# Optimization experiments

Hardware: AMD Instinct MI355X
Metric: run time of the kernel (lower is better)

## Reference

```python
import jax, jax.numpy as jnp
import numpy as np
from jax import lax

WS = 7  # window_size
PAD = WS // 2


def _gaussian_window(window_size, channel, sigma=1.5):
    x = np.arange(window_size, dtype=np.float64)
    g = np.exp(-((x - window_size // 2) ** 2) / (2.0 * sigma ** 2))
    g = g / g.sum()
    w2 = np.outer(g, g).astype(np.float32)  # (ws, ws)
    w = np.broadcast_to(w2[None, None], (channel, 1, window_size, window_size))
    return jnp.asarray(np.ascontiguousarray(w))


def setup_inputs() -> dict:
    key = jax.random.key(0)
    k1, k2, k3 = jax.random.split(key, 3)
    shape = (16, 1, 1024, 1024)
    img1 = jax.random.uniform(k1, shape, dtype=jnp.float32)
    img2 = jax.random.uniform(k2, shape, dtype=jnp.float32)
    img3 = jax.random.uniform(k3, shape, dtype=jnp.float32)
    window = _gaussian_window(WS, channel=1)  # (1,1,7,7) depthwise Gaussian
    return {"img1": img1, "img2": img2, "img3": img3, "window": window}


def _dwconv(x, window, channel):
    # depthwise conv2d, SAME-style padding = ws//2, groups = channel
    return lax.conv_general_dilated(
        x, window, window_strides=(1, 1), padding=[(PAD, PAD), (PAD, PAD)],
        dimension_numbers=("NCHW", "OIHW", "NCHW"), feature_group_count=channel)


def reference(img1, img2, img3, window):
    channel = img1.shape[1]
    conv = lambda x: _dwconv(x, window, channel)

    mu1 = conv(img1)
    mu2 = conv(img2)
    mu3 = conv(img3)

    sigma1_sq = conv(img1 * img1) - mu1 * mu1
    sigma2_sq = conv(img2 * img2) - mu2 * mu2
    sigma3_sq = conv(img3 * img3) - mu3 * mu3
    sigma12 = conv(img1 * img2) - mu1 * mu2
    sigma13 = conv(img1 * img3) - mu1 * mu3

    C2 = 0.03 ** 2
    ssim_map_12 = (2.0 * sigma12 + C2) / (sigma1_sq + sigma2_sq + C2)
    ssim_map_13 = (2.0 * sigma13 + C2) / (sigma1_sq + sigma3_sq + C2)

    # size_average=True branch
    ssim_map = jnp.where(mu2 > mu3, ssim_map_12, ssim_map_13)
    return jnp.mean(ssim_map)
```

## Files before the change

kernel.cpp:

```cpp
#include <hip/hip_runtime.h>

typedef float v2f __attribute__((ext_vector_type(2)));

#define W 1024
#define H 1024
#define NB 16
#define TX 32
#define TY 18
#define HR 24
#define NTH 192
#define YBLK ((H + TY - 1) / TY)
#define RSTRIDE (8 * TX)

__global__ __launch_bounds__(NTH, 4) void ssim_main(
    const float* __restrict__ img1, const float* __restrict__ img2,
    const float* __restrict__ img3, const float* __restrict__ win,
    float* __restrict__ partial)
{
    __shared__ __align__(16) float hbuf[HR * RSTRIDE];
    __shared__ float wavesum[3];

    const int tid = threadIdx.x;
    const int x0  = blockIdx.x * TX;
    const int ys0 = blockIdx.y * TY;
    const size_t imoff = (size_t)blockIdx.z * (size_t)(W * H);
    const float* p1 = img1 + imoff;
    const float* p2 = img2 + imoff;
    const float* p3 = img3 + imoff;

    float g[7];
    {
        const float inv = 1.0f / sqrtf(win[24]);
        #pragma unroll
        for (int j = 0; j < 7; ++j) g[j] = win[21 + j] * inv;
    }

    {
        const int br  = tid >> 3;
        const int bc0 = (tid & 7) << 2;
        const int gy  = ys0 + br - 3;
        const int gx0 = x0 + bc0 - 4;
        const bool xfast = (gx0 >= 0) & (gx0 + 12 <= W);

        v2f accA[8], accB[8];
        #pragma unroll
        for (int ch = 0; ch < 8; ++ch) { accA[ch] = (v2f)0.0f; accB[ch] = (v2f)0.0f; }

        if ((gy >= 0) & (gy < H)) {
            const size_t rowoff = (size_t)gy * W;
            float V1[12], V2[12], V3[12];
            if (xfast) {
                const float* q1 = p1 + rowoff + gx0;
                const float* q2 = p2 + rowoff + gx0;
                const float* q3 = p3 + rowoff + gx0;
                *(float4*)&V1[0] = *(const float4*)(q1);
                *(float4*)&V1[4] = *(const float4*)(q1 + 4);
                *(float4*)&V1[8] = *(const float4*)(q1 + 8);
                *(float4*)&V2[0] = *(const float4*)(q2);
                *(float4*)&V2[4] = *(const float4*)(q2 + 4);
                *(float4*)&V2[8] = *(const float4*)(q2 + 8);
                *(float4*)&V3[0] = *(const float4*)(q3);
                *(float4*)&V3[4] = *(const float4*)(q3 + 4);
                *(float4*)&V3[8] = *(const float4*)(q3 + 8);
            } else {
                #pragma unroll
                for (int c = 0; c < 12; ++c) {
                    const int x = gx0 + c;
                    const bool ok = (x >= 0) & (x < W);
                    const size_t off = rowoff + x;
                    V1[c] = ok ? p1[off] : 0.0f;
                    V2[c] = ok ? p2[off] : 0.0f;
                    V3[c] = ok ? p3[off] : 0.0f;
                }
            }

            v2f gp[8];
            gp[0] = (v2f){g[0], 0.0f};
            #pragma unroll
            for (int m = 2; m <= 7; ++m) gp[m - 1] = (v2f){g[m - 1], g[m - 2]};
            gp[7] = (v2f){0.0f, g[6]};

            #pragma unroll
            for (int m = 1; m <= 8; ++m) {
                const v2f w = gp[m - 1];
                const float vA1 = V1[m], vA2 = V2[m], vA3 = V3[m];
                const float vB1 = V1[m + 2], vB2 = V2[m + 2], vB3 = V3[m + 2];
                v2f t;
                t = w * vA1; accA[0] += t; accA[3] += t * vA1; accA[6] += t * vA2; accA[7] += t * vA3;
                t = w * vA2; accA[1] += t; accA[4] += t * vA2;
                t = w * vA3; accA[2] += t; accA[5] += t * vA3;
                t = w * vB1; accB[0] += t; accB[3] += t * vB1; accB[6] += t * vB2; accB[7] += t * vB3;
                t = w * vB2; accB[1] += t; accB[4] += t * vB2;
                t = w * vB3; accB[2] += t; accB[5] += t * vB3;
            }
        }
        const int wbase = br * RSTRIDE + bc0;
        #pragma unroll
        for (int ch = 0; ch < 8; ++ch) {
            *(v2f*)&hbuf[wbase + ch * TX]     = accA[ch];
            *(v2f*)&hbuf[wbase + ch * TX + 2] = accB[ch];
        }
    }
    __syncthreads();

    const int tx = tid & 31;
    const int rg = tid >> 5;
    const int r0 = rg * 3;

    v2f s[4][3];
    #pragma unroll
    for (int cp = 0; cp < 4; ++cp)
        #pragma unroll
        for (int j = 0; j < 3; ++j) s[cp][j] = (v2f)0.0f;

    int base = r0 * RSTRIDE + tx;
    #pragma unroll
    for (int dy = 0; dy < 9; ++dy) {
        v2f p[4];
        #pragma unroll
        for (int cp = 0; cp < 4; ++cp) {
            p[cp].x = hbuf[base + cp * 64];
            p[cp].y = hbuf[base + cp * 64 + 32];
        }
        #pragma unroll
        for (int j = 0; j < 3; ++j) {
            const int dd = dy - j;
            if (dd >= 0 && dd < 7) {
                const float wg = g[dd];
                #pragma unroll
                for (int cp = 0; cp < 4; ++cp) s[cp][j] += wg * p[cp];
            }
        }
        base += RSTRIDE;
    }

    float lsum = 0.0f;
    #pragma unroll
    for (int j = 0; j < 3; ++j) {
        if (ys0 + r0 + j < H) {
            const float mu1 = s[0][j].x, mu2 = s[0][j].y;
            const float mu3 = s[1][j].x, E11 = s[1][j].y;
            const float E22 = s[2][j].x, E33 = s[2][j].y;
            const float E12 = s[3][j].x, E13 = s[3][j].y;
            const float sig1  = E11 - mu1 * mu1;
            const float sig2  = E22 - mu2 * mu2;
            const float sig3  = E33 - mu3 * mu3;
            const float sig12 = E12 - mu1 * mu2;
            const float sig13 = E13 - mu1 * mu3;
            const float C2 = 9.0e-4f;
            const float m12 = (2.0f * sig12 + C2) * __builtin_amdgcn_rcpf(sig1 + sig2 + C2);
            const float m13 = (2.0f * sig13 + C2) * __builtin_amdgcn_rcpf(sig1 + sig3 + C2);
            lsum += (mu2 > mu3) ? m12 : m13;
        }
    }

    #pragma unroll
    for (int o = 32; o > 0; o >>= 1) lsum += __shfl_down(lsum, o, 64);
    if ((tid & 63) == 0) wavesum[tid >> 6] = lsum;
    __syncthreads();
    if (tid == 0) {
        partial[((size_t)blockIdx.z * gridDim.y + blockIdx.y) * gridDim.x + blockIdx.x] =
            wavesum[0] + wavesum[1] + wavesum[2];
    }
}

__global__ __launch_bounds__(256) void ssim_reduce(
    const float* __restrict__ partial, float* __restrict__ out, int n)
{
    __shared__ double sh[256];
    const int tid = threadIdx.x;
    double s = 0.0;
    for (int i = tid; i < n; i += 256) s += (double)partial[i];
    sh[tid] = s;
    __syncthreads();
    for (int o = 128; o > 0; o >>= 1) {
        if (tid < o) sh[tid] += sh[tid + o];
        __syncthreads();
    }
    if (tid == 0) out[0] = (float)(sh[0] / (double)((size_t)NB * W * H));
}

extern "C" void kernel_launch(void* const* d_in, const int* in_sizes, int n_in,
                              void* d_out, int out_size, void* d_ws, size_t ws_size,
                              hipStream_t stream) {
    const float* img1 = (const float*)d_in[0];
    const float* img2 = (const float*)d_in[1];
    const float* img3 = (const float*)d_in[2];
    const float* win  = (const float*)d_in[3];
    float* out = (float*)d_out;
    float* partial = (float*)d_ws;

    dim3 grid(W / TX, YBLK, NB);
    ssim_main<<<grid, NTH, 0, stream>>>(img1, img2, img3, win, partial);

    const int nblk = (W / TX) * YBLK * NB;
    ssim_reduce<<<1, 256, 0, stream>>>(partial, out, nblk);
}
```

Measured before the change: 128.4 us.

## March blocks down a tall column strip, reusing the vertical halo across steps

Each block now handles a 32x128 strip in four 32-row steps instead of one 32x18 tile. It computes horizontal convolutions only for new rows and copies the 6-row halo inside shared memory between steps. This removes the heavy recomputation and reloading of halo rows: the old tiles spent 24 horizontal rows per 18 output rows, the new scheme about 38 per 128. The cost is extra syncs per step, a serial loop with less latency hiding, fewer blocks in the grid, and a larger shared buffer per block.

```diff
diff --git a/kernel.cpp b/kernel.cpp
--- a/kernel.cpp
+++ b/kernel.cpp
@@ -6,23 +6,81 @@
 #define H 1024
 #define NB 16
 #define TX 32
-#define TY 18
-#define HR 24
-#define NTH 192
-#define YBLK ((H + TY - 1) / TY)
+#define STEP 32
+#define NSTEP 4
+#define YSEG (STEP * NSTEP)
+#define BR 38
+#define NTH 256
 #define RSTRIDE (8 * TX)
+
+__device__ __forceinline__ void hconv_task(
+    const float* __restrict__ p1, const float* __restrict__ p2,
+    const float* __restrict__ p3, int gy, int gx0, bool xfast,
+    const v2f* __restrict__ gp, float* __restrict__ dst )
+{
+    v2f accA[8], accB[8];
+    #pragma unroll
+    for (int ch = 0; ch < 8; ++ch) { accA[ch] = (v2f)0.0f; accB[ch] = (v2f)0.0f; }
+
+    if ((gy >= 0) & (gy < H)) {
+        const size_t rowoff = (size_t)gy * W;
+        float V1[12], V2[12], V3[12];
+        if (xfast) {
+            const float* q1 = p1 + rowoff + gx0;
+            const float* q2 = p2 + rowoff + gx0;
+            const float* q3 = p3 + rowoff + gx0;
+            *(float4*)&V1[0] = *(const float4*)(q1);
+            *(float4*)&V1[4] = *(const float4*)(q1 + 4);
+            *(float4*)&V1[8] = *(const float4*)(q1 + 8);
+            *(float4*)&V2[0] = *(const float4*)(q2);
+            *(float4*)&V2[4] = *(const float4*)(q2 + 4);
+            *(float4*)&V2[8] = *(const float4*)(q2 + 8);
+            *(float4*)&V3[0] = *(const float4*)(q3);
+            *(float4*)&V3[4] = *(const float4*)(q3 + 4);
+            *(float4*)&V3[8] = *(const float4*)(q3 + 8);
+        } else {
+            #pragma unroll
+            for (int c = 0; c < 12; ++c) {
+                const int x = gx0 + c;
+                const bool ok = (x >= 0) & (x < W);
+                const size_t off = rowoff + x;
+                V1[c] = ok ? p1[off] : 0.0f;
+                V2[c] = ok ? p2[off] : 0.0f;
+                V3[c] = ok ? p3[off] : 0.0f;
+            }
+        }
+        #pragma unroll
+        for (int m = 1; m <= 8; ++m) {
+            const v2f w = gp[m - 1];
+            const float vA1 = V1[m], vA2 = V2[m], vA3 = V3[m];
+            const float vB1 = V1[m + 2], vB2 = V2[m + 2], vB3 = V3[m + 2];
+            v2f t;
+            t = w * vA1; accA[0] += t; accA[3] += t * vA1; accA[6] += t * vA2; accA[7] += t * vA3;
+            t = w * vA2; accA[1] += t; accA[4] += t * vA2;
+            t = w * vA3; accA[2] += t; accA[5] += t * vA3;
+            t = w * vB1; accB[0] += t; accB[3] += t * vB1; accB[6] += t * vB2; accB[7] += t * vB3;
+            t = w * vB2; accB[1] += t; accB[4] += t * vB2;
+            t = w * vB3; accB[2] += t; accB[5] += t * vB3;
+        }
+    }
+    #pragma unroll
+    for (int ch = 0; ch < 8; ++ch) {
+        *(v2f*)(dst + ch * TX)     = accA[ch];
+        *(v2f*)(dst + ch * TX + 2) = accB[ch];
+    }
+}
 
 __global__ __launch_bounds__(NTH, 4) void ssim_main(
     const float* __restrict__ img1, const float* __restrict__ img2,
     const float* __restrict__ img3, const float* __restrict__ win,
     float* __restrict__ partial)
 {
-    __shared__ __align__(16) float hbuf[HR * RSTRIDE];
-    __shared__ float wavesum[3];
+    __shared__ __align__(16) float hbuf[BR * RSTRIDE];
+    __shared__ float wavesum[4];
 
     const int tid = threadIdx.x;
     const int x0  = blockIdx.x * TX;
-    const int ys0 = blockIdx.y * TY;
+    const int ys0 = blockIdx.y * YSEG;
     const size_t imoff = (size_t)blockIdx.z * (size_t)(W * H);
     const float* p1 = img1 + imoff;
     const float* p2 = img2 + imoff;
@@ -34,114 +92,67 @@
         #pragma unroll
         for (int j = 0; j < 7; ++j) g[j] = win[21 + j] * inv;
     }
-
-    {
-        const int br  = tid >> 3;
-        const int bc0 = (tid & 7) << 2;
-        const int gy  = ys0 + br - 3;
-        const int gx0 = x0 + bc0 - 4;
-        const bool xfast = (gx0 >= 0) & (gx0 + 12 <= W);
-
-        v2f accA[8], accB[8];
-        #pragma unroll
-        for (int ch = 0; ch < 8; ++ch) { accA[ch] = (v2f)0.0f; accB[ch] = (v2f)0.0f; }
-
-        if ((gy >= 0) & (gy < H)) {
-            const size_t rowoff = (size_t)gy * W;
-            float V1[12], V2[12], V3[12];
-            if (xfast) {
-                const float* q1 = p1 + rowoff + gx0;
-                const float* q2 = p2 + rowoff + gx0;
-                const float* q3 = p3 + rowoff + gx0;
-                *(float4*)&V1[0] = *(const float4*)(q1);
-                *(float4*)&V1[4] = *(const float4*)(q1 + 4);
-                *(float4*)&V1[8] = *(const float4*)(q1 + 8);
-                *(float4*)&V2[0] = *(const float4*)(q2);
-                *(float4*)&V2[4] = *(const float4*)(q2 + 4);
-                *(float4*)&V2[8] = *(const float4*)(q2 + 8);
-                *(float4*)&V3[0] = *(const float4*)(q3);
-                *(float4*)&V3[4] = *(const float4*)(q3 + 4);
-                *(float4*)&V3[8] = *(const float4*)(q3 + 8);
-            } else {
-                #pragma unroll
-                for (int c = 0; c < 12; ++c) {
-                    const int x = gx0 + c;
-                    const bool ok = (x >= 0) & (x < W);
-                    const size_t off = rowoff + x;
-                    V1[c] = ok ? p1[off] : 0.0f;
-                    V2[c] = ok ? p2[off] : 0.0f;
-                    V3[c] = ok ? p3[off] : 0.0f;
+    v2f gp[8];
+    gp[0] = (v2f){g[0], 0.0f};
+    #pragma unroll
+    for (int m = 2; m <= 7; ++m) gp[m - 1] = (v2f){g[m - 1], g[m - 2]};
+    gp[7] = (v2f){0.0f, g[6]};
+
+    const int br  = tid >> 3;
+    const int bc0 = (tid & 7) << 2;
+    const int gx0 = x0 + bc0 - 4;
+    const bool xfast = (gx0 >= 0) & (gx0 + 12 <= W);
+
+    if (tid < 48) {
+        const int pr  = tid >> 3;
+        const int pc0 = (tid & 7) << 2;
+        const int pgx0 = x0 + pc0 - 4;
+        const bool pxf = (pgx0 >= 0) & (pgx0 + 12 <= W);
+        hconv_task(p1, p2, p3, ys0 - 3 + pr, pgx0, pxf, gp, &hbuf[pr * RSTRIDE + pc0]);
+    }
+
+    const int tx = tid & 31;
+    const int r0 = (tid >> 5) << 2;
+
+    float lsum = 0.0f;
+
+    for (int s = 0; s < NSTEP; ++s) {
+        hconv_task(p1, p2, p3, ys0 + s * STEP + 3 + br, gx0, xfast, gp,
+                   &hbuf[(6 + br) * RSTRIDE + bc0]);
+        __syncthreads();
+
+        v2f sv[4][4];
+        #pragma unroll
+        for (int cp = 0; cp < 4; ++cp)
+            #pragma unroll
+            for (int j = 0; j < 4; ++j) sv[cp][j] = (v2f)0.0f;
+
+        int base = r0 * RSTRIDE + tx;
+        #pragma unroll
+        for (int dy = 0; dy < 10; ++dy) {
+            v2f p[4];
+            #pragma unroll
+            for (int cp = 0; cp < 4; ++cp) {
+                p[cp].x = hbuf[base + cp * 64];
+                p[cp].y = hbuf[base + cp * 64 + 32];
+            }
+            #pragma unroll
+            for (int j = 0; j < 4; ++j) {
+                const int dd = dy - j;
+                if (dd >= 0 && dd < 7) {
+                    const float wg = g[dd];
+                    #pragma unroll
+                    for (int cp = 0; cp < 4; ++cp) sv[cp][j] += wg * p[cp];
                 }
             }
-
-            v2f gp[8];
-            gp[0] = (v2f){g[0], 0.0f};
-            #pragma unroll
-            for (int m = 2; m <= 7; ++m) gp[m - 1] = (v2f){g[m - 1], g[m - 2]};
-            gp[7] = (v2f){0.0f, g[6]};
-
-            #pragma unroll
-            for (int m = 1; m <= 8; ++m) {
-                const v2f w = gp[m - 1];
-                const float vA1 = V1[m], vA2 = V2[m], vA3 = V3[m];
-                const float vB1 = V1[m + 2], vB2 = V2[m + 2], vB3 = V3[m + 2];
-                v2f t;
-                t = w * vA1; accA[0] += t; accA[3] += t * vA1; accA[6] += t * vA2; accA[7] += t * vA3;
-                t = w * vA2; accA[1] += t; accA[4] += t * vA2;
-                t = w * vA3; accA[2] += t; accA[5] += t * vA3;
-                t = w * vB1; accB[0] += t; accB[3] += t * vB1; accB[6] += t * vB2; accB[7] += t * vB3;
-                t = w * vB2; accB[1] += t; accB[4] += t * vB2;
-                t = w * vB3; accB[2] += t; accB[5] += t * vB3;
-            }
-        }
-        const int wbase = br * RSTRIDE + bc0;
-        #pragma unroll
-        for (int ch = 0; ch < 8; ++ch) {
-            *(v2f*)&hbuf[wbase + ch * TX]     = accA[ch];
-            *(v2f*)&hbuf[wbase + ch * TX + 2] = accB[ch];
-        }
-    }
-    __syncthreads();
-
-    const int tx = tid & 31;
-    const int rg = tid >> 5;
-    const int r0 = rg * 3;
-
-    v2f s[4][3];
-    #pragma unroll
-    for (int cp = 0; cp < 4; ++cp)
-        #pragma unroll
-        for (int j = 0; j < 3; ++j) s[cp][j] = (v2f)0.0f;
-
-    int base = r0 * RSTRIDE + tx;
-    #pragma unroll
-    for (int dy = 0; dy < 9; ++dy) {
-        v2f p[4];
-        #pragma unroll
-        for (int cp = 0; cp < 4; ++cp) {
-            p[cp].x = hbuf[base + cp * 64];
-            p[cp].y = hbuf[base + cp * 64 + 32];
-        }
-        #pragma unroll
-        for (int j = 0; j < 3; ++j) {
-            const int dd = dy - j;
-            if (dd >= 0 && dd < 7) {
-                const float wg = g[dd];
-                #pragma unroll
-                for (int cp = 0; cp < 4; ++cp) s[cp][j] += wg * p[cp];
-            }
-        }
-        base += RSTRIDE;
-    }
-
-    float lsum = 0.0f;
-    #pragma unroll
-    for (int j = 0; j < 3; ++j) {
-        if (ys0 + r0 + j < H) {
-            const float mu1 = s[0][j].x, mu2 = s[0][j].y;
-            const float mu3 = s[1][j].x, E11 = s[1][j].y;
-            const float E22 = s[2][j].x, E33 = s[2][j].y;
-            const float E12 = s[3][j].x, E13 = s[3][j].y;
+            base += RSTRIDE;
+        }
+        #pragma unroll
+        for (int j = 0; j < 4; ++j) {
+            const float mu1 = sv[0][j].x, mu2 = sv[0][j].y;
+            const float mu3 = sv[1][j].x, E11 = sv[1][j].y;
+            const float E22 = sv[2][j].x, E33 = sv[2][j].y;
+            const float E12 = sv[3][j].x, E13 = sv[3][j].y;
             const float sig1  = E11 - mu1 * mu1;
             const float sig2  = E22 - mu2 * mu2;
             const float sig3  = E33 - mu3 * mu3;
@@ -152,6 +163,18 @@
             const float m13 = (2.0f * sig13 + C2) * __builtin_amdgcn_rcpf(sig1 + sig3 + C2);
             lsum += (mu2 > mu3) ? m12 : m13;
         }
+        __syncthreads();
+
+        if (s < NSTEP - 1) {
+            const int co = tid * 6;
+            const v2f a = *(const v2f*)&hbuf[32 * RSTRIDE + co];
+            const v2f b = *(const v2f*)&hbuf[32 * RSTRIDE + co + 2];
+            const v2f c = *(const v2f*)&hbuf[32 * RSTRIDE + co + 4];
+            *(v2f*)&hbuf[co]     = a;
+            *(v2f*)&hbuf[co + 2] = b;
+            *(v2f*)&hbuf[co + 4] = c;
+            __syncthreads();
+        }
     }
 
     #pragma unroll
@@ -159,8 +182,8 @@
     if ((tid & 63) == 0) wavesum[tid >> 6] = lsum;
     __syncthreads();
     if (tid == 0) {
-        partial[((size_t)blockIdx.z * gridDim.y + blockIdx.y) * gridDim.x + blockIdx.x] =
-            wavesum[0] + wavesum[1] + wavesum[2];
+        const float t = (wavesum[0] + wavesum[1]) + (wavesum[2] + wavesum[3]);
+        partial[((size_t)blockIdx.z * gridDim.y + blockIdx.y) * gridDim.x + blockIdx.x] = t;
     }
 }
 
@@ -190,9 +213,9 @@
     float* out = (float*)d_out;
     float* partial = (float*)d_ws;
 
-    dim3 grid(W / TX, YBLK, NB);
+    dim3 grid(W / TX, H / YSEG, NB);
     ssim_main<<<grid, NTH, 0, stream>>>(img1, img2, img3, win, partial);
 
-    const int nblk = (W / TX) * YBLK * NB;
+    const int nblk = (W / TX) * (H / YSEG) * NB;
     ssim_reduce<<<1, 256, 0, stream>>>(partial, out, nblk);
 }
```

After: 254.6 us. 1.98x slower.
